# Kernel optimization log

Hardware: AMD Instinct MI355X
Metric: run time of the kernel (lower is better)

Reference implementation:

```python
import jax, jax.numpy as jnp
import numpy as np

N, I, O, ITERS = 65536, 16, 16, 3
EPS = 1e-8


def hamilton(q, r):
    # Hamilton quaternion product, broadcasting over leading dims; q, r: [..., 4]
    w1, x1, y1, z1 = jnp.moveaxis(q, -1, 0)
    w2, x2, y2, z2 = jnp.moveaxis(r, -1, 0)
    return jnp.stack([
        w1 * w2 - x1 * x2 - y1 * y2 - z1 * z2,
        w1 * x2 + x1 * w2 + y1 * z2 - z1 * y2,
        w1 * y2 - x1 * z2 + y1 * w2 + z1 * x2,
        w1 * z2 + x1 * y2 - y1 * x2 + z1 * w2,
    ], axis=-1)


def squash(s):
    # capsule squash nonlinearity along the last (quaternion) axis
    n2 = jnp.sum(s * s, axis=-1, keepdims=True)
    return s * (n2 / (1.0 + n2)) / jnp.sqrt(n2 + EPS)


def setup_inputs() -> dict:
    key = jax.random.key(0)
    ks = jax.random.split(key, 7)
    return {
        "x": jax.random.normal(ks[0], (N, I, 4), dtype=jnp.float32),
        "quats": jax.random.normal(ks[1], (O, I, 4), dtype=jnp.float32),
        "scale": jax.random.normal(ks[2], (O, I, 1), dtype=jnp.float32),
        "trans": jax.random.normal(ks[3], (O, I, 3), dtype=jnp.float32),
        "bias": jax.random.normal(ks[4], (O,), dtype=jnp.float32),
        "beta": jax.random.normal(ks[5], (O,), dtype=jnp.float32),
        "alpha": jax.random.normal(ks[6], (O,), dtype=jnp.float32),
    }


def reference(x, quats, scale, trans, bias, beta, alpha):
    # normalize learned quaternions to unit rotations: [O, I, 4]
    qn = quats / jnp.sqrt(jnp.sum(quats * quats, axis=-1, keepdims=True) + EPS)
    # votes: rotate each input capsule pose by each (out,in) quaternion -> [N, O, I, 4]
    votes = scale[None] * hamilton(qn[None], x[:, None])
    # translate the vector (imaginary) part of the vote quaternion
    votes = jnp.concatenate([votes[..., :1], votes[..., 1:] + trans[None]], axis=-1)

    b = jnp.zeros((x.shape[0], O, I), dtype=x.dtype)  # routing logits
    for _ in range(ITERS):
        c = jax.nn.softmax(b, axis=1)                    # couple over output caps
        s = jnp.einsum('noi,noid->nod', c, votes)        # weighted vote sum [N,O,4]
        v = squash(s)                                    # output poses [N,O,4]
        b = b + jnp.einsum('nod,noid->noi', v, votes)    # agreement update

    norm_s = jnp.sqrt(jnp.sum(s * s, axis=-1) + EPS)     # [N, O]
    a = jax.nn.sigmoid(beta * norm_s + alpha + bias)     # output activations [N, O]
    return v * a[..., None]                              # activation-scaled poses [N,O,4]
```

## Files before the change

### kernel.cpp

```cpp
#include <hip/hip_runtime.h>
#include <math.h>

#define EPSQ 1e-8f
#define LOG2E 1.4426950408889634f
#define TILES_PER_BLOCK 4

typedef float f2 __attribute__((ext_vector_type(2)));

__device__ __forceinline__ float rcp_fast(float x) { return __builtin_amdgcn_rcpf(x); }
__device__ __forceinline__ float rsq_fast(float x) { return __builtin_amdgcn_rsqf(x); }
__device__ __forceinline__ f2 pk_fma(f2 a, f2 b, f2 c) { return __builtin_elementwise_fma(a, b, c); }

#define DPP_F(x, ctrl) \
    __int_as_float(__builtin_amdgcn_update_dpp(0, __float_as_int(x), (ctrl), 0xF, 0xF, true))

__device__ __forceinline__ float allsum16(float v) {
    v += DPP_F(v, 0xB1);
    v += DPP_F(v, 0x4E);
    v += DPP_F(v, 0x124);
    v += DPP_F(v, 0x128);
    return v;
}

__global__ __launch_bounds__(256, 4) void caps_kernel(
    const float* __restrict__ x,
    const float* __restrict__ quats,
    const float* __restrict__ scale,
    const float* __restrict__ trans,
    const float* __restrict__ bias,
    const float* __restrict__ beta,
    const float* __restrict__ alpha,
    float* __restrict__ out,
    int tiles_total)
{
    __shared__ __align__(16) float qs[16][16][4];
    __shared__ __align__(16) float tr[16][16][4];
    __shared__ __align__(16) float xs[2][16][68];

    const int tid = threadIdx.x;
    const int o   = tid & 15;
    const int ln  = tid >> 4;

    {
        const int o2 = tid & 15, i2 = tid >> 4;
        const int pidx = o2 * 16 + i2;
        const float4 q = ((const float4*)quats)[pidx];
        const float sc = scale[pidx];
        const float qn2 = q.x*q.x + q.y*q.y + q.z*q.z + q.w*q.w;
        const float f = sc * rsq_fast(qn2 + EPSQ);
        qs[i2][o2][0] = q.x * f;
        qs[i2][o2][1] = q.y * f;
        qs[i2][o2][2] = q.z * f;
        qs[i2][o2][3] = q.w * f;
        tr[i2][o2][0] = 0.0f;
        tr[i2][o2][1] = trans[pidx*3 + 0];
        tr[i2][o2][2] = trans[pidx*3 + 1];
        tr[i2][o2][3] = trans[pidx*3 + 2];
    }
    const float beta_o = beta[o];
    const float ab_o   = alpha[o] + bias[o];

    size_t tile = blockIdx.x;
    {
        const float4 xv = ((const float4*)x)[tile * 256 + tid];
        *(float4*)&xs[0][tid >> 4][(tid & 15) * 4] = xv;
    }
    __syncthreads();

    #pragma unroll
    for (int t = 0; t < TILES_PER_BLOCK; ++t) {
        float4 xnext;
        const size_t ntile = tile + gridDim.x;
        if (t < TILES_PER_BLOCK - 1)
            xnext = ((const float4*)x)[ntile * 256 + tid];

        const int buf = t & 1;

        f2 vwx[16], vyz[16];
        #pragma unroll
        for (int i = 0; i < 16; ++i) {
            const float4 q4 = *(const float4*)&qs[i][o][0];
            const float4 t4 = *(const float4*)&tr[i][o][0];
            const float4 x4 = *(const float4*)&xs[buf][ln][i * 4];
            f2 a, b2;
            a = pk_fma(f2{ q4.x,  q4.x}, f2{x4.x, x4.y}, f2{t4.x, t4.y});
            a = pk_fma(f2{-q4.y,  q4.y}, f2{x4.y, x4.x}, a);
            a = pk_fma(f2{-q4.z,  q4.z}, f2{x4.z, x4.w}, a);
            a = pk_fma(f2{-q4.w, -q4.w}, f2{x4.w, x4.z}, a);
            b2 = pk_fma(f2{ q4.x,  q4.x}, f2{x4.z, x4.w}, f2{t4.z, t4.w});
            b2 = pk_fma(f2{-q4.y,  q4.y}, f2{x4.w, x4.z}, b2);
            b2 = pk_fma(f2{ q4.z, -q4.z}, f2{x4.x, x4.y}, b2);
            b2 = pk_fma(f2{ q4.w,  q4.w}, f2{x4.y, x4.x}, b2);
            vwx[i] = a; vyz[i] = b2;
        }

        f2 vlwx, vlyz, v0wx, v0yz;

        {
            f2 uwx = f2{0.f, 0.f}, uyz = f2{0.f, 0.f};
            #pragma unroll
            for (int i = 0; i < 16; ++i) { uwx += vwx[i]; uyz += vyz[i]; }
            f2 d = uwx * uwx;
            d = pk_fma(uyz, uyz, d);
            const float n2 = (d.x + d.y) * (1.0f / 256.0f);
            const float fq = n2 * rcp_fast(1.f + n2) * rsq_fast(n2 + EPSQ) * 0.0625f;
            v0wx = uwx * fq; v0yz = uyz * fq;
            vlwx = v0wx * LOG2E; vlyz = v0yz * LOG2E;
        }

        f2 s_wx, s_yz, vowx, voyz;
        #pragma unroll
        for (int it = 1; it < 3; ++it) {
            f2 snwx = f2{0.f, 0.f}, snyz = f2{0.f, 0.f};
            #pragma unroll
            for (int i = 0; i < 16; ++i) {
                f2 d2 = vlwx * vwx[i];
                d2 = pk_fma(vlyz, vyz[i], d2);
                const float e  = __builtin_amdgcn_exp2f(d2.x + d2.y);
                const float se = allsum16(e);
                const float c  = e * rcp_fast(se);
                snwx = pk_fma(f2{c, c}, vwx[i], snwx);
                snyz = pk_fma(f2{c, c}, vyz[i], snyz);
            }
            s_wx = snwx; s_yz = snyz;
            const float n2 = snwx.x*snwx.x + snwx.y*snwx.y + snyz.x*snyz.x + snyz.y*snyz.y;
            const float fq = n2 * rcp_fast(1.f + n2) * rsq_fast(n2 + EPSQ);
            vowx = snwx * fq; voyz = snyz * fq;
            if (it == 1) {
                vlwx = (v0wx + vowx) * LOG2E;
                vlyz = (v0yz + voyz) * LOG2E;
            }
        }

        const float n2f = s_wx.x*s_wx.x + s_wx.y*s_wx.y + s_yz.x*s_yz.x + s_yz.y*s_yz.y;
        const float norm_s = sqrtf(n2f + EPSQ);
        const float tgt = beta_o * norm_s + ab_o;
        const float aAct = rcp_fast(1.f + __builtin_amdgcn_exp2f(-tgt * LOG2E));
        float4 ov;
        ov.x = vowx.x * aAct; ov.y = vowx.y * aAct;
        ov.z = voyz.x * aAct; ov.w = voyz.y * aAct;
        ((float4*)out)[tile * 256 + tid] = ov;

        if (t < TILES_PER_BLOCK - 1) {
            *(float4*)&xs[buf ^ 1][tid >> 4][(tid & 15) * 4] = xnext;
            __syncthreads();
            tile = ntile;
        }
    }
}

extern "C" void kernel_launch(void* const* d_in, const int* in_sizes, int n_in,
                              void* d_out, int out_size, void* d_ws, size_t ws_size,
                              hipStream_t stream) {
    const float* x     = (const float*)d_in[0];
    const float* quats = (const float*)d_in[1];
    const float* scale = (const float*)d_in[2];
    const float* trans = (const float*)d_in[3];
    const float* bias  = (const float*)d_in[4];
    const float* beta  = (const float*)d_in[5];
    const float* alpha = (const float*)d_in[6];
    float* out = (float*)d_out;

    const int N = in_sizes[0] / 64;
    const int tiles = N / 16;
    const int grid = tiles / TILES_PER_BLOCK;
    caps_kernel<<<grid, 256, 0, stream>>>(x, quats, scale, trans, bias, beta, alpha,
                                          out, tiles);
}
```

Measured before the change: 99.22 us.

## Process one tile per block and emit Hamilton votes via inline packed-FMA asm

Removes the multi-tile persistent loop with double-buffered x prefetch, so each block now handles a single 16-sample tile and the grid has one block per tile. The quaternion vote computation is replaced by inline v_pk_fma_f32 assembly that uses op_sel and neg modifiers to avoid building swizzled and negated operand vectors. The aim is to cut VALU instruction count and register pressure and to get more blocks in flight. The cost is that the per-block normalisation of quats into shared memory is now repeated once for every tile, and the load-compute overlap from prefetching is lost.

```diff
diff --git a/kernel.cpp b/kernel.cpp
--- a/kernel.cpp
+++ b/kernel.cpp
@@ -3,9 +3,9 @@
 
 #define EPSQ 1e-8f
 #define LOG2E 1.4426950408889634f
-#define TILES_PER_BLOCK 4
 
 typedef float f2 __attribute__((ext_vector_type(2)));
+typedef float f4 __attribute__((ext_vector_type(4)));
 
 __device__ __forceinline__ float rcp_fast(float x) { return __builtin_amdgcn_rcpf(x); }
 __device__ __forceinline__ float rsq_fast(float x) { return __builtin_amdgcn_rsqf(x); }
@@ -22,6 +22,20 @@
     return v;
 }
 
+__device__ __forceinline__ void hamilton_pk(f2 q01, f2 q23, f2 p01, f2 p23,
+                                            f2 ta, f2 tb, f2& a, f2& b2) {
+    asm("v_pk_fma_f32 %0, %2, %3, %4 op_sel:[0,0,0] op_sel_hi:[0,1,1]\n\t"
+        "v_pk_fma_f32 %0, %2, %3, %0 op_sel:[1,1,0] op_sel_hi:[1,0,1] neg_lo:[1,0,0]\n\t"
+        "v_pk_fma_f32 %0, %5, %6, %0 op_sel:[0,0,0] op_sel_hi:[0,1,1] neg_lo:[1,0,0]\n\t"
+        "v_pk_fma_f32 %0, %5, %6, %0 op_sel:[1,1,0] op_sel_hi:[1,0,1] neg_lo:[1,0,0] neg_hi:[1,0,0]\n\t"
+        "v_pk_fma_f32 %1, %2, %6, %7 op_sel:[0,0,0] op_sel_hi:[0,1,1]\n\t"
+        "v_pk_fma_f32 %1, %2, %6, %1 op_sel:[1,1,0] op_sel_hi:[1,0,1] neg_lo:[1,0,0]\n\t"
+        "v_pk_fma_f32 %1, %5, %3, %1 op_sel:[0,0,0] op_sel_hi:[0,1,1] neg_hi:[1,0,0]\n\t"
+        "v_pk_fma_f32 %1, %5, %3, %1 op_sel:[1,1,0] op_sel_hi:[1,0,1]"
+        : "=&v"(a), "=&v"(b2)
+        : "v"(q01), "v"(p01), "v"(ta), "v"(q23), "v"(p23), "v"(tb));
+}
+
 __global__ __launch_bounds__(256, 4) void caps_kernel(
     const float* __restrict__ x,
     const float* __restrict__ quats,
@@ -30,12 +44,11 @@
     const float* __restrict__ bias,
     const float* __restrict__ beta,
     const float* __restrict__ alpha,
-    float* __restrict__ out,
-    int tiles_total)
+    float* __restrict__ out)
 {
     __shared__ __align__(16) float qs[16][16][4];
     __shared__ __align__(16) float tr[16][16][4];
-    __shared__ __align__(16) float xs[2][16][68];
+    __shared__ __align__(16) float xs[16][68];
 
     const int tid = threadIdx.x;
     const int o   = tid & 15;
@@ -57,96 +70,67 @@
         tr[i2][o2][2] = trans[pidx*3 + 1];
         tr[i2][o2][3] = trans[pidx*3 + 2];
     }
-    const float beta_o = beta[o];
-    const float ab_o   = alpha[o] + bias[o];
-
-    size_t tile = blockIdx.x;
     {
-        const float4 xv = ((const float4*)x)[tile * 256 + tid];
-        *(float4*)&xs[0][tid >> 4][(tid & 15) * 4] = xv;
+        const float4 xv = ((const float4*)x)[(size_t)blockIdx.x * 256 + tid];
+        *(float4*)&xs[tid >> 4][(tid & 15) * 4] = xv;
     }
     __syncthreads();
 
+    f2 vwx[16], vyz[16];
     #pragma unroll
-    for (int t = 0; t < TILES_PER_BLOCK; ++t) {
-        float4 xnext;
-        const size_t ntile = tile + gridDim.x;
-        if (t < TILES_PER_BLOCK - 1)
-            xnext = ((const float4*)x)[ntile * 256 + tid];
+    for (int i = 0; i < 16; ++i) {
+        const f4 q4 = *(const f4*)&qs[i][o][0];
+        const f4 t4 = *(const f4*)&tr[i][o][0];
+        const f4 x4 = *(const f4*)&xs[ln][i * 4];
+        hamilton_pk(q4.lo, q4.hi, x4.lo, x4.hi, t4.lo, t4.hi, vwx[i], vyz[i]);
+    }
 
-        const int buf = t & 1;
+    f2 vlwx, vlyz, v0wx, v0yz;
 
-        f2 vwx[16], vyz[16];
+    {
+        f2 uwx = f2{0.f, 0.f}, uyz = f2{0.f, 0.f};
+        #pragma unroll
+        for (int i = 0; i < 16; ++i) { uwx += vwx[i]; uyz += vyz[i]; }
+        f2 d = uwx * uwx;
+        d = pk_fma(uyz, uyz, d);
+        const float n2 = (d.x + d.y) * (1.0f / 256.0f);
+        const float fq = n2 * rcp_fast(1.f + n2) * rsq_fast(n2 + EPSQ) * 0.0625f;
+        v0wx = uwx * fq; v0yz = uyz * fq;
+        vlwx = v0wx * LOG2E; vlyz = v0yz * LOG2E;
+    }
+
+    f2 s_wx, s_yz, vowx, voyz;
+    #pragma unroll
+    for (int it = 1; it < 3; ++it) {
+        f2 snwx = f2{0.f, 0.f}, snyz = f2{0.f, 0.f};
         #pragma unroll
         for (int i = 0; i < 16; ++i) {
-            const float4 q4 = *(const float4*)&qs[i][o][0];
-            const float4 t4 = *(const float4*)&tr[i][o][0];
-            const float4 x4 = *(const float4*)&xs[buf][ln][i * 4];
-            f2 a, b2;
-            a = pk_fma(f2{ q4.x,  q4.x}, f2{x4.x, x4.y}, f2{t4.x, t4.y});
-            a = pk_fma(f2{-q4.y,  q4.y}, f2{x4.y, x4.x}, a);
-            a = pk_fma(f2{-q4.z,  q4.z}, f2{x4.z, x4.w}, a);
-            a = pk_fma(f2{-q4.w, -q4.w}, f2{x4.w, x4.z}, a);
-            b2 = pk_fma(f2{ q4.x,  q4.x}, f2{x4.z, x4.w}, f2{t4.z, t4.w});
-            b2 = pk_fma(f2{-q4.y,  q4.y}, f2{x4.w, x4.z}, b2);
-            b2 = pk_fma(f2{ q4.z, -q4.z}, f2{x4.x, x4.y}, b2);
-            b2 = pk_fma(f2{ q4.w,  q4.w}, f2{x4.y, x4.x}, b2);
-            vwx[i] = a; vyz[i] = b2;
+            f2 d2 = vlwx * vwx[i];
+            d2 = pk_fma(vlyz, vyz[i], d2);
+            const float e  = __builtin_amdgcn_exp2f(d2.x + d2.y);
+            const float se = allsum16(e);
+            const float c  = e * rcp_fast(se);
+            snwx = pk_fma(f2{c, c}, vwx[i], snwx);
+            snyz = pk_fma(f2{c, c}, vyz[i], snyz);
         }
-
-        f2 vlwx, vlyz, v0wx, v0yz;
-
-        {
-            f2 uwx = f2{0.f, 0.f}, uyz = f2{0.f, 0.f};
-            #pragma unroll
-            for (int i = 0; i < 16; ++i) { uwx += vwx[i]; uyz += vyz[i]; }
-            f2 d = uwx * uwx;
-            d = pk_fma(uyz, uyz, d);
-            const float n2 = (d.x + d.y) * (1.0f / 256.0f);
-            const float fq = n2 * rcp_fast(1.f + n2) * rsq_fast(n2 + EPSQ) * 0.0625f;
-            v0wx = uwx * fq; v0yz = uyz * fq;
-            vlwx = v0wx * LOG2E; vlyz = v0yz * LOG2E;
-        }
-
-        f2 s_wx, s_yz, vowx, voyz;
-        #pragma unroll
-        for (int it = 1; it < 3; ++it) {
-            f2 snwx = f2{0.f, 0.f}, snyz = f2{0.f, 0.f};
-            #pragma unroll
-            for (int i = 0; i < 16; ++i) {
-                f2 d2 = vlwx * vwx[i];
-                d2 = pk_fma(vlyz, vyz[i], d2);
-                const float e  = __builtin_amdgcn_exp2f(d2.x + d2.y);
-                const float se = allsum16(e);
-                const float c  = e * rcp_fast(se);
-                snwx = pk_fma(f2{c, c}, vwx[i], snwx);
-                snyz = pk_fma(f2{c, c}, vyz[i], snyz);
-            }
-            s_wx = snwx; s_yz = snyz;
-            const float n2 = snwx.x*snwx.x + snwx.y*snwx.y + snyz.x*snyz.x + snyz.y*snyz.y;
-            const float fq = n2 * rcp_fast(1.f + n2) * rsq_fast(n2 + EPSQ);
-            vowx = snwx * fq; voyz = snyz * fq;
-            if (it == 1) {
-                vlwx = (v0wx + vowx) * LOG2E;
-                vlyz = (v0yz + voyz) * LOG2E;
-            }
-        }
-
-        const float n2f = s_wx.x*s_wx.x + s_wx.y*s_wx.y + s_yz.x*s_yz.x + s_yz.y*s_yz.y;
-        const float norm_s = sqrtf(n2f + EPSQ);
-        const float tgt = beta_o * norm_s + ab_o;
-        const float aAct = rcp_fast(1.f + __builtin_amdgcn_exp2f(-tgt * LOG2E));
-        float4 ov;
-        ov.x = vowx.x * aAct; ov.y = vowx.y * aAct;
-        ov.z = voyz.x * aAct; ov.w = voyz.y * aAct;
-        ((float4*)out)[tile * 256 + tid] = ov;
-
-        if (t < TILES_PER_BLOCK - 1) {
-            *(float4*)&xs[buf ^ 1][tid >> 4][(tid & 15) * 4] = xnext;
-            __syncthreads();
-            tile = ntile;
+        s_wx = snwx; s_yz = snyz;
+        const float n2 = snwx.x*snwx.x + snwx.y*snwx.y + snyz.x*snyz.x + snyz.y*snyz.y;
+        const float fq = n2 * rcp_fast(1.f + n2) * rsq_fast(n2 + EPSQ);
+        vowx = snwx * fq; voyz = snyz * fq;
+        if (it == 1) {
+            vlwx = (v0wx + vowx) * LOG2E;
+            vlyz = (v0yz + voyz) * LOG2E;
         }
     }
+
+    const float n2f = s_wx.x*s_wx.x + s_wx.y*s_wx.y + s_yz.x*s_yz.x + s_yz.y*s_yz.y;
+    const float norm_s = sqrtf(n2f + EPSQ);
+    const float tgt = beta[o] * norm_s + alpha[o] + bias[o];
+    const float aAct = rcp_fast(1.f + __builtin_amdgcn_exp2f(-tgt * LOG2E));
+    float4 ov;
+    ov.x = vowx.x * aAct; ov.y = vowx.y * aAct;
+    ov.z = voyz.x * aAct; ov.w = voyz.y * aAct;
+    ((float4*)out)[(size_t)blockIdx.x * 256 + tid] = ov;
 }
 
 extern "C" void kernel_launch(void* const* d_in, const int* in_sizes, int n_in,
@@ -162,8 +146,5 @@
     float* out = (float*)d_out;
 
     const int N = in_sizes[0] / 64;
-    const int tiles = N / 16;
-    const int grid = tiles / TILES_PER_BLOCK;
-    caps_kernel<<<grid, 256, 0, stream>>>(x, quats, scale, trans, bias, beta, alpha,
-                                          out, tiles);
+    caps_kernel<<<N / 16, 256, 0, stream>>>(x, quats, scale, trans, bias, beta, alpha, out);
 }
```

Result: no change. 97.43 us (-1.8%).
